# Kernel optimization log

Measured on AMD Instinct MI355X. Metric: run time of the kernel, lower is better.

The kernel has to match this reference:

```python
import jax, jax.numpy as jnp
import numpy as np
import math

EMBED_DIM = 1024
BATCH = 4
SEQ = 2048


def setup_inputs() -> dict:
    key = jax.random.key(0)
    ks = jax.random.split(key, 7)
    d = EMBED_DIM
    s = 1.0 / math.sqrt(d)
    x = jax.random.normal(ks[0], (BATCH, SEQ, d), dtype=jnp.float32)
    Wq = jax.random.normal(ks[1], (d, d), dtype=jnp.float32) * s
    Wk = jax.random.normal(ks[2], (d, d), dtype=jnp.float32) * s
    Wv = jax.random.normal(ks[3], (d, d), dtype=jnp.float32) * s
    bq = jax.random.normal(ks[4], (d,), dtype=jnp.float32) * 0.01
    bk = jax.random.normal(ks[5], (d,), dtype=jnp.float32) * 0.01
    bv = jax.random.normal(ks[6], (d,), dtype=jnp.float32) * 0.01
    return {"x": x, "Wq": Wq, "bq": bq, "Wk": Wk, "bk": bk, "Wv": Wv, "bv": bv}


def reference(x, Wq, bq, Wk, bk, Wv, bv):
    # q/k/v: [B, S, D] linear projections (weights stored as [in, out])
    q = jnp.einsum('bsd,de->bse', x, Wq) + bq
    k = jnp.einsum('bsd,de->bse', x, Wk) + bk
    v = jnp.einsum('bsd,de->bse', x, Wv) + bv
    scale = jnp.sqrt(jnp.asarray(x.shape[-1], dtype=x.dtype))
    # full O(S^2) score matrix, as in the original (non-fused) attention
    attn_scores = jnp.einsum('bqd,bkd->bqk', q, k) / scale
    attn_probs = jax.nn.softmax(attn_scores, axis=-1)
    # lxa.strassen(attn_probs, v) is a (Strassen) matmul: same math as matmul
    return jnp.einsum('bqk,bkd->bqd', attn_probs, v)
```

## Files before the change

### kernel.cpp

```cpp
#include <hip/hip_runtime.h>
#include <stdint.h>

#define SEQ 2048
#define DIM 1024
#define NB 4
#define MTOT (NB*SEQ)
#define QKVN (3*DIM)

typedef __attribute__((ext_vector_type(8))) short short8;
typedef __attribute__((ext_vector_type(4))) float f32x4;

__device__ __forceinline__ unsigned short f2b(float f) {
    union { float f; unsigned int u; } v; v.f = f;
    return (unsigned short)((v.u + 0x7FFFu + ((v.u >> 16) & 1u)) >> 16);
}

__device__ __forceinline__ void gload_lds16(const unsigned short* g, unsigned short* l) {
    __builtin_amdgcn_global_load_lds(
        (const __attribute__((address_space(1))) void*)g,
        (__attribute__((address_space(3))) void*)l, 16, 0, 0);
}

__device__ __forceinline__ short8 ds128(unsigned addr) {
    short8 r;
    asm volatile("ds_read_b128 %0, %1" : "=v"(r) : "v"(addr));
    return r;
}

#define FENCE_BARRIER do { asm volatile("" ::: "memory"); \
    __builtin_amdgcn_s_barrier(); asm volatile("" ::: "memory"); } while (0)

__device__ __forceinline__ int xcd_swz(int bid, int nwg) {
    if (nwg & 7) return bid;
    return (bid & 7) * (nwg >> 3) + (bid >> 3);
}


__global__ __launch_bounds__(256)
void cast_kernel(const float* __restrict__ in, unsigned short* __restrict__ out, int nchunk) {
    int i = blockIdx.x * 256 + threadIdx.x;
    if (i >= nchunk) return;
    float4 a = ((const float4*)in)[i*2];
    float4 b = ((const float4*)in)[i*2+1];
    union { unsigned short u[8]; uint4 v; } r;
    r.u[0]=f2b(a.x); r.u[1]=f2b(a.y); r.u[2]=f2b(a.z); r.u[3]=f2b(a.w);
    r.u[4]=f2b(b.x); r.u[5]=f2b(b.y); r.u[6]=f2b(b.z); r.u[7]=f2b(b.w);
    ((uint4*)out)[i] = r.v;
}

__global__ __launch_bounds__(256)
void transpose_cast_f32(const float* __restrict__ in, unsigned short* __restrict__ out, int R, int C) {
    __shared__ unsigned short tile[64][66];
    int tpc = C >> 6;
    int tr = (blockIdx.x / tpc) << 6;
    int tc = (blockIdx.x % tpc) << 6;
    int t = threadIdx.x;
    #pragma unroll
    for (int i = 0; i < 16; i++) {
        int idx = t + i*256;
        int r = idx >> 6, c = idx & 63;
        tile[r][c] = f2b(in[(size_t)(tr + r)*C + tc + c]);
    }
    __syncthreads();
    #pragma unroll
    for (int i = 0; i < 16; i++) {
        int idx = t + i*256;
        int r = idx >> 6, c = idx & 63;
        out[(size_t)(tc + r)*R + tr + c] = tile[c][r];
    }
}

__global__ __launch_bounds__(256)
void transpose_b16(const unsigned short* __restrict__ in0, size_t sIn, int ldin,
                   unsigned short* __restrict__ out0, size_t sOut, int ldout, int tpc) {
    const unsigned short* in = in0 + sIn * blockIdx.y;
    unsigned short* out = out0 + sOut * blockIdx.y;
    __shared__ unsigned short tile[64][66];
    int tr = ((int)blockIdx.x / tpc) << 6;
    int tc = ((int)blockIdx.x % tpc) << 6;
    int t = threadIdx.x;
    #pragma unroll
    for (int i = 0; i < 16; i++) {
        int idx = t + i*256;
        int r = idx >> 6, c = idx & 63;
        tile[r][c] = in[(size_t)(tr + r)*ldin + tc + c];
    }
    __syncthreads();
    #pragma unroll
    for (int i = 0; i < 16; i++) {
        int idx = t + i*256;
        int r = idx >> 6, c = idx & 63;
        out[(size_t)(tc + r)*ldout + tr + c] = tile[c][r];
    }
}

__global__ __launch_bounds__(256)
void bias_concat(const float* __restrict__ bq, const float* __restrict__ bk,
                 const float* __restrict__ bv, float* __restrict__ o) {
    int i = blockIdx.x*256 + threadIdx.x;
    float v = (i < DIM) ? bq[i] : ((i < 2*DIM) ? bk[i-DIM] : bv[i-2*DIM]);
    o[i] = v;
}


__device__ __forceinline__ void stage1(const unsigned short* __restrict__ Xb, int ldx,
                                       unsigned short* dstBase, int h, int k0,
                                       int tid, int wid) {
    int srow = tid >> 3;
    int scol = ((tid & 7) ^ (srow & 7)) << 3;
    const unsigned short* g = Xb + (size_t)(h*128 + srow)*ldx + k0 + scol;
    unsigned short* d = dstBase + h*8192 + wid*512;
    gload_lds16(g, d);
    gload_lds16(g + (size_t)64*ldx, d + 4096);
}

#define LDA_Q(BUF, QM) do { _Pragma("unroll") for (int mf = 0; mf < 4; ++mf) { \
    fa[mf][0] = ds128(As0 + (BUF)*32768u + (QM)*16384u + aRow + mf*2048u + c0); \
    fa[mf][1] = ds128(As0 + (BUF)*32768u + (QM)*16384u + aRow + mf*2048u + c1); } } while (0)

#define LDB_Q(BUF, QN) do { _Pragma("unroll") for (int nf = 0; nf < 2; ++nf) { \
    fb[nf][0] = ds128(Bs0 + (BUF)*32768u + (QN)*16384u + bRow + nf*2048u + c0); \
    fb[nf][1] = ds128(Bs0 + (BUF)*32768u + (QN)*16384u + bRow + nf*2048u + c1); } } while (0)

#define MMA_PH(QM, QN) do { \
    asm volatile("s_waitcnt lgkmcnt(0)" ::: "memory"); \
    __builtin_amdgcn_sched_barrier(0); \
    __builtin_amdgcn_s_setprio(1); \
    _Pragma("unroll") for (int mf = 0; mf < 4; ++mf) \
      _Pragma("unroll") for (int nf = 0; nf < 2; ++nf) \
        _Pragma("unroll") for (int ks = 0; ks < 2; ++ks) \
          acc[QM][QN][mf][nf] = __builtin_amdgcn_mfma_f32_16x16x32_bf16( \
              fa[mf][ks], fb[nf][ks], acc[QM][QN][mf][nf], 0, 0, 0); \
    __builtin_amdgcn_s_setprio(0); \
} while (0)

template<int MODE>
__global__ __launch_bounds__(512, 2)
void gemm8p(const unsigned short* __restrict__ A, int lda, size_t sA,
            const unsigned short* __restrict__ Bt, int ldb, size_t sB,
            const float* __restrict__ bias,
            void* __restrict__ Cout, int ldc, size_t sC,
            int N, int K)
{
    __shared__ __align__(16) unsigned short As[2][16384];
    __shared__ __align__(16) unsigned short Bs[2][16384];
    int nbn = N >> 8;
    int bid = xcd_swz((int)blockIdx.x, (int)gridDim.x);
    int bm = bid / nbn, bn = bid % nbn;
    int bz = blockIdx.y;
    int tid = threadIdx.x;
    int lane = tid & 63;
    int wid  = tid >> 6;
    int wm = (wid >> 2) & 1;
    int wn = wid & 3;
    int rlo = lane & 15;
    int shi = lane >> 4;

    unsigned As0 = (unsigned)(uintptr_t)&As[0][0];
    unsigned Bs0 = (unsigned)(uintptr_t)&Bs[0][0];
    unsigned c0 = (unsigned)(((shi     ^ rlo) & 7) * 16);
    unsigned c1 = (unsigned)((((4+shi) ^ rlo) & 7) * 16);
    unsigned aRow = (unsigned)((wm*64 + rlo) * 128);
    unsigned bRow = (unsigned)((wn*32 + rlo) * 128);

    f32x4 acc[2][2][4][2];
    #pragma unroll
    for (int a = 0; a < 2; a++)
        #pragma unroll
        for (int b = 0; b < 2; b++)
            #pragma unroll
            for (int c = 0; c < 4; c++)
                #pragma unroll
                for (int d = 0; d < 2; d++)
                    acc[a][b][c][d] = (f32x4){0.f,0.f,0.f,0.f};

    const unsigned short* Ab = A + sA*bz + (size_t)(bm*256)*lda;
    const unsigned short* Bb = Bt + sB*bz + (size_t)(bn*256)*ldb;

    stage1(Ab, lda, &As[0][0], 0, 0,  tid, wid);
    stage1(Bb, ldb, &Bs[0][0], 0, 0,  tid, wid);
    stage1(Ab, lda, &As[0][0], 1, 0,  tid, wid);
    stage1(Bb, ldb, &Bs[0][0], 1, 0,  tid, wid);
    stage1(Ab, lda, &As[1][0], 0, 64, tid, wid);
    stage1(Bb, ldb, &Bs[1][0], 1, 64, tid, wid);
    stage1(Ab, lda, &As[1][0], 1, 64, tid, wid);
    asm volatile("s_waitcnt vmcnt(6)" ::: "memory");
    FENCE_BARRIER;

    short8 fa[4][2], fb[2][2];
    int nt = K >> 6;
    int nit = nt >> 1;

    for (int it = 0; it < nit; ++it) {
        int kO  = (2*it + 1) << 6;
        int kE2 = (2*it + 2 < nt) ? (2*it + 2) << 6 : 0;
        int kO2 = (2*it + 3 < nt) ? (2*it + 3) << 6 : 0;

        LDA_Q(0, 0); LDB_Q(0, 0);
        stage1(Bb, ldb, &Bs[1][0], 0, kO, tid, wid);
        FENCE_BARRIER; MMA_PH(0, 0); FENCE_BARRIER;
        LDB_Q(0, 1);
        stage1(Ab, lda, &As[0][0], 0, kE2, tid, wid);
        FENCE_BARRIER; MMA_PH(0, 1); FENCE_BARRIER;
        LDA_Q(0, 1);
        stage1(Bb, ldb, &Bs[0][0], 1, kE2, tid, wid);
        FENCE_BARRIER; MMA_PH(1, 1); FENCE_BARRIER;
        LDB_Q(0, 0);
        stage1(Ab, lda, &As[0][0], 1, kE2, tid, wid);
        asm volatile("s_waitcnt vmcnt(6)" ::: "memory");
        FENCE_BARRIER; MMA_PH(1, 0); FENCE_BARRIER;
        LDA_Q(1, 0); LDB_Q(1, 0);
        stage1(Bb, ldb, &Bs[0][0], 0, kE2, tid, wid);
        FENCE_BARRIER; MMA_PH(0, 0); FENCE_BARRIER;
        LDB_Q(1, 1);
        stage1(Ab, lda, &As[1][0], 0, kO2, tid, wid);
        FENCE_BARRIER; MMA_PH(0, 1); FENCE_BARRIER;
        LDA_Q(1, 1);
        stage1(Bb, ldb, &Bs[1][0], 1, kO2, tid, wid);
        FENCE_BARRIER; MMA_PH(1, 1); FENCE_BARRIER;
        LDB_Q(1, 0);
        stage1(Ab, lda, &As[1][0], 1, kO2, tid, wid);
        asm volatile("s_waitcnt vmcnt(6)" ::: "memory");
        FENCE_BARRIER; MMA_PH(1, 0); FENCE_BARRIER;
    }

    asm volatile("s_waitcnt vmcnt(0)" ::: "memory");

    int r0 = shi << 2;
    unsigned short* Cu = (unsigned short*)Cout + sC*bz;
    float* Cf = (float*)Cout + sC*bz;
    #pragma unroll
    for (int qm = 0; qm < 2; ++qm)
        #pragma unroll
        for (int qn = 0; qn < 2; ++qn)
            #pragma unroll
            for (int mf = 0; mf < 4; ++mf)
                #pragma unroll
                for (int nf = 0; nf < 2; ++nf) {
                    int col = bn*256 + qn*128 + wn*32 + nf*16 + rlo;
                    float badd = (MODE == 0) ? bias[col] : 0.f;
                    #pragma unroll
                    for (int r = 0; r < 4; ++r) {
                        int row = bm*256 + qm*128 + wm*64 + mf*16 + r0 + r;
                        float v = acc[qm][qn][mf][nf][r];
                        if (MODE == 0) Cu[(size_t)row*ldc + col] = f2b(v + badd);
                        else           Cf[(size_t)row*ldc + col] = v;
                    }
                }
}

__global__ __launch_bounds__(256, 2)
void gemm_nt_pv(const unsigned short* __restrict__ A, int lda, size_t sA,
                const unsigned short* __restrict__ Bt, int ldb, size_t sB,
                float* __restrict__ Cout, int ldc, size_t sC,
                int N, int K)
{
    __shared__ __align__(16) unsigned short As[128][64];
    __shared__ __align__(16) unsigned short Bs[128][64];
    int nbn = N >> 7;
    int bid = xcd_swz((int)blockIdx.x, (int)gridDim.x);
    int bm = bid / nbn;
    int bn = bid % nbn;
    int bz = blockIdx.y;
    int tid = threadIdx.x;
    int lane = tid & 63;
    int wid  = tid >> 6;
    int wm = (wid >> 1) * 64, wn = (wid & 1) * 64;
    int lr = lane & 15;
    int lk = (lane >> 4) * 8;
    int srow = lane >> 3;
    int scol = (lane & 7) * 8;

    f32x4 acc[4][4];
    #pragma unroll
    for (int i = 0; i < 4; i++)
        #pragma unroll
        for (int j = 0; j < 4; j++) acc[i][j] = (f32x4){0.f,0.f,0.f,0.f};

    const unsigned short* Ab = A + sA*bz + (size_t)(bm*128)*lda;
    const unsigned short* Bb = Bt + sB*bz + (size_t)(bn*128)*ldb;

    for (int k0 = 0; k0 < K; k0 += 64) {
        #pragma unroll
        for (int r = 0; r < 4; r++) {
            int rowg = r*32 + wid*8;
            gload_lds16(Ab + (size_t)(rowg + srow)*lda + k0 + scol, &As[rowg][0]);
            gload_lds16(Bb + (size_t)(rowg + srow)*ldb + k0 + scol, &Bs[rowg][0]);
        }
        __syncthreads();
        #pragma unroll
        for (int ks = 0; ks < 2; ks++) {
            short8 af[4], bfr[4];
            #pragma unroll
            for (int mf = 0; mf < 4; mf++)
                af[mf] = *(const short8*)&As[wm + mf*16 + lr][ks*32 + lk];
            #pragma unroll
            for (int nf = 0; nf < 4; nf++)
                bfr[nf] = *(const short8*)&Bs[wn + nf*16 + lr][ks*32 + lk];
            #pragma unroll
            for (int mf = 0; mf < 4; mf++)
                #pragma unroll
                for (int nf = 0; nf < 4; nf++)
                    acc[mf][nf] = __builtin_amdgcn_mfma_f32_16x16x32_bf16(af[mf], bfr[nf], acc[mf][nf], 0, 0, 0);
        }
        __syncthreads();
    }

    int r0 = (lane >> 4) << 2;
    float* Cf = Cout + sC*bz;
    #pragma unroll
    for (int mf = 0; mf < 4; mf++)
        #pragma unroll
        for (int nf = 0; nf < 4; nf++) {
            int col = bn*128 + wn + nf*16 + lr;
            #pragma unroll
            for (int r = 0; r < 4; r++) {
                int row = bm*128 + wm + mf*16 + r0 + r;
                Cf[(size_t)row*ldc + col] = acc[mf][nf][r];
            }
        }
}

__global__ __launch_bounds__(256)
void softmax_kernel(float* __restrict__ S, float scl) {
    int row = blockIdx.x;
    float* srow = S + (size_t)row * SEQ;
    int t = threadIdx.x;
    float4 v0 = ((const float4*)srow)[t*2];
    float4 v1 = ((const float4*)srow)[t*2+1];
    float x[8] = {v0.x*scl,v0.y*scl,v0.z*scl,v0.w*scl,v1.x*scl,v1.y*scl,v1.z*scl,v1.w*scl};
    float m = fmaxf(fmaxf(fmaxf(x[0],x[1]),fmaxf(x[2],x[3])),
                    fmaxf(fmaxf(x[4],x[5]),fmaxf(x[6],x[7])));
    #pragma unroll
    for (int off = 32; off; off >>= 1) m = fmaxf(m, __shfl_xor(m, off));
    __shared__ float redm[4], reds[4];
    int w = t >> 6;
    if ((t & 63) == 0) redm[w] = m;
    __syncthreads();
    m = fmaxf(fmaxf(redm[0], redm[1]), fmaxf(redm[2], redm[3]));
    float e[8]; float s = 0.f;
    #pragma unroll
    for (int i = 0; i < 8; i++) { e[i] = __expf(x[i] - m); s += e[i]; }
    #pragma unroll
    for (int off = 32; off; off >>= 1) s += __shfl_xor(s, off);
    if ((t & 63) == 0) reds[w] = s;
    __syncthreads();
    float inv = 1.0f / (reds[0]+reds[1]+reds[2]+reds[3]);
    union { unsigned short u[8]; uint4 v; } r;
    #pragma unroll
    for (int i = 0; i < 8; i++) r.u[i] = f2b(e[i] * inv);
    ((uint4*)srow)[t] = r.v;
}

extern "C" void kernel_launch(void* const* d_in, const int* in_sizes, int n_in,
                              void* d_out, int out_size, void* d_ws, size_t ws_size,
                              hipStream_t stream)
{
    (void)in_sizes; (void)n_in; (void)out_size;
    const float* x  = (const float*)d_in[0];
    const float* Wq = (const float*)d_in[1];
    const float* bq = (const float*)d_in[2];
    const float* Wk = (const float*)d_in[3];
    const float* bk = (const float*)d_in[4];
    const float* Wv = (const float*)d_in[5];
    const float* bv = (const float*)d_in[6];
    float* out = (float*)d_out;

    unsigned short* qkv = (unsigned short*)d_ws;
    unsigned short* vt  = qkv + (size_t)MTOT*QKVN;
    float* biasc = (float*)(vt + (size_t)NB*DIM*SEQ);
    char* ovl = (char*)biasc + 65536;
    unsigned short* xb    = (unsigned short*)ovl;
    unsigned short* wqkvt = xb + (size_t)MTOT*DIM;
    float* scores = (float*)ovl;

    size_t base = (size_t)MTOT*QKVN*2 + (size_t)NB*DIM*SEQ*2 + 65536;
    int bpp = 1;
    if (base + 4*(size_t)SEQ*SEQ*4 <= ws_size) bpp = 4;
    else if (base + 2*(size_t)SEQ*SEQ*4 <= ws_size) bpp = 2;

    cast_kernel<<<MTOT*DIM/8/256, 256, 0, stream>>>(x, xb, MTOT*DIM/8);
    transpose_cast_f32<<<256, 256, 0, stream>>>(Wq, wqkvt,             DIM, DIM);
    transpose_cast_f32<<<256, 256, 0, stream>>>(Wk, wqkvt + DIM*DIM,   DIM, DIM);
    transpose_cast_f32<<<256, 256, 0, stream>>>(Wv, wqkvt + 2*DIM*DIM, DIM, DIM);
    bias_concat<<<QKVN/256, 256, 0, stream>>>(bq, bk, bv, biasc);

    gemm8p<0><<<dim3((MTOT/256)*(QKVN/256)), 512, 0, stream>>>(
        xb, DIM, 0, wqkvt, DIM, 0, biasc, qkv, QKVN, 0, QKVN, DIM);

    transpose_b16<<<dim3((SEQ/64)*(DIM/64), NB), 256, 0, stream>>>(
        qkv + 2*DIM, (size_t)SEQ*QKVN, QKVN, vt, (size_t)DIM*SEQ, SEQ, DIM/64);

    const float scl = 1.0f / 32.0f;
    for (int p = 0; p < NB; p += bpp) {
        const unsigned short* qp = qkv + (size_t)p*SEQ*QKVN;
        gemm8p<1><<<dim3((SEQ/256)*(SEQ/256), bpp), 512, 0, stream>>>(
            qp,       QKVN, (size_t)SEQ*QKVN,
            qp + DIM, QKVN, (size_t)SEQ*QKVN,
            nullptr, scores, SEQ, (size_t)SEQ*SEQ, SEQ, DIM);
        softmax_kernel<<<bpp*SEQ, 256, 0, stream>>>(scores, scl);
        gemm_nt_pv<<<dim3((SEQ/128)*(DIM/128), bpp), 256, 0, stream>>>(
            (const unsigned short*)scores, 2*SEQ, (size_t)SEQ*2*SEQ,
            vt + (size_t)p*DIM*SEQ,        SEQ,   (size_t)DIM*SEQ,
            out + (size_t)p*SEQ*DIM, DIM, (size_t)SEQ*DIM, DIM, SEQ);
    }
}
```

Before: 193.1 us.

## Software-pipeline LDS fragment reads with MFMA phases using double register buffers

```diff
diff --git a/kernel.cpp b/kernel.cpp
--- a/kernel.cpp
+++ b/kernel.cpp
@@ -114,24 +114,25 @@
     gload_lds16(g + (size_t)64*ldx, d + 4096);
 }
 
-#define LDA_Q(BUF, QM) do { _Pragma("unroll") for (int mf = 0; mf < 4; ++mf) { \
-    fa[mf][0] = ds128(As0 + (BUF)*32768u + (QM)*16384u + aRow + mf*2048u + c0); \
-    fa[mf][1] = ds128(As0 + (BUF)*32768u + (QM)*16384u + aRow + mf*2048u + c1); } } while (0)
-
-#define LDB_Q(BUF, QN) do { _Pragma("unroll") for (int nf = 0; nf < 2; ++nf) { \
-    fb[nf][0] = ds128(Bs0 + (BUF)*32768u + (QN)*16384u + bRow + nf*2048u + c0); \
-    fb[nf][1] = ds128(Bs0 + (BUF)*32768u + (QN)*16384u + bRow + nf*2048u + c1); } } while (0)
-
-#define MMA_PH(QM, QN) do { \
-    asm volatile("s_waitcnt lgkmcnt(0)" ::: "memory"); \
+#define RD_A(DST, BUF, QM) do { _Pragma("unroll") for (int mf = 0; mf < 4; ++mf) { \
+    DST[mf][0] = ds128(As0 + (BUF)*32768u + (QM)*16384u + aRow + mf*2048u + c0);   \
+    DST[mf][1] = ds128(As0 + (BUF)*32768u + (QM)*16384u + aRow + mf*2048u + c1); } } while (0)
+
+#define RD_B(DST, BUF, QN) do { _Pragma("unroll") for (int nf = 0; nf < 2; ++nf) { \
+    DST[nf][0] = ds128(Bs0 + (BUF)*32768u + (QN)*16384u + bRow + nf*2048u + c0);   \
+    DST[nf][1] = ds128(Bs0 + (BUF)*32768u + (QN)*16384u + bRow + nf*2048u + c1); } } while (0)
+
+#define MMA16(FA, FB, QM, QN) do { \
     __builtin_amdgcn_sched_barrier(0); \
     __builtin_amdgcn_s_setprio(1); \
     _Pragma("unroll") for (int mf = 0; mf < 4; ++mf) \
       _Pragma("unroll") for (int nf = 0; nf < 2; ++nf) \
         _Pragma("unroll") for (int ks = 0; ks < 2; ++ks) \
           acc[QM][QN][mf][nf] = __builtin_amdgcn_mfma_f32_16x16x32_bf16( \
-              fa[mf][ks], fb[nf][ks], acc[QM][QN][mf][nf], 0, 0, 0); \
+              FA[mf][ks], FB[nf][ks], acc[QM][QN][mf][nf], 0, 0, 0); \
     __builtin_amdgcn_s_setprio(0); \
+    asm volatile("s_waitcnt lgkmcnt(0)" ::: "memory"); \
+    __builtin_amdgcn_sched_barrier(0); \
 } while (0)
 
 template<int MODE>
@@ -177,6 +178,11 @@
     const unsigned short* Ab = A + sA*bz + (size_t)(bm*256)*lda;
     const unsigned short* Bb = Bt + sB*bz + (size_t)(bn*256)*ldb;
 
+    short8 faA[4][2], faB[4][2];
+    short8 fb0X[2][2];
+    short8 fb0Y[2][2];
+    short8 fb1[2][2];
+
     stage1(Ab, lda, &As[0][0], 0, 0,  tid, wid);
     stage1(Bb, ldb, &Bs[0][0], 0, 0,  tid, wid);
     stage1(Ab, lda, &As[0][0], 1, 0,  tid, wid);
@@ -184,44 +190,57 @@
     stage1(Ab, lda, &As[1][0], 0, 64, tid, wid);
     stage1(Bb, ldb, &Bs[1][0], 1, 64, tid, wid);
     stage1(Ab, lda, &As[1][0], 1, 64, tid, wid);
+    stage1(Bb, ldb, &Bs[1][0], 0, 64, tid, wid);
+    __builtin_amdgcn_sched_barrier(0);
     asm volatile("s_waitcnt vmcnt(6)" ::: "memory");
     FENCE_BARRIER;
-
-    short8 fa[4][2], fb[2][2];
+    RD_A(faA, 0, 0); RD_B(fb0X, 0, 0);
+    __builtin_amdgcn_sched_barrier(0);
+    asm volatile("s_waitcnt lgkmcnt(0)" ::: "memory");
+    __builtin_amdgcn_sched_barrier(0);
+    FENCE_BARRIER;
+
     int nt = K >> 6;
     int nit = nt >> 1;
 
     for (int it = 0; it < nit; ++it) {
-        int kO  = (2*it + 1) << 6;
         int kE2 = (2*it + 2 < nt) ? (2*it + 2) << 6 : 0;
         int kO2 = (2*it + 3 < nt) ? (2*it + 3) << 6 : 0;
 
-        LDA_Q(0, 0); LDB_Q(0, 0);
-        stage1(Bb, ldb, &Bs[1][0], 0, kO, tid, wid);
-        FENCE_BARRIER; MMA_PH(0, 0); FENCE_BARRIER;
-        LDB_Q(0, 1);
+        RD_B(fb1, 0, 1);
+        MMA16(faA, fb0X, 0, 0);
         stage1(Ab, lda, &As[0][0], 0, kE2, tid, wid);
-        FENCE_BARRIER; MMA_PH(0, 1); FENCE_BARRIER;
-        LDA_Q(0, 1);
+        FENCE_BARRIER;
+        RD_A(faB, 0, 1);
+        MMA16(faA, fb1, 0, 1);
         stage1(Bb, ldb, &Bs[0][0], 1, kE2, tid, wid);
-        FENCE_BARRIER; MMA_PH(1, 1); FENCE_BARRIER;
-        LDB_Q(0, 0);
+        FENCE_BARRIER;
+        MMA16(faB, fb1, 1, 1);
         stage1(Ab, lda, &As[0][0], 1, kE2, tid, wid);
+        __builtin_amdgcn_sched_barrier(0);
         asm volatile("s_waitcnt vmcnt(6)" ::: "memory");
-        FENCE_BARRIER; MMA_PH(1, 0); FENCE_BARRIER;
-        LDA_Q(1, 0); LDB_Q(1, 0);
+        FENCE_BARRIER;
+        RD_A(faA, 1, 0); RD_B(fb0Y, 1, 0);
+        MMA16(faB, fb0X, 1, 0);
         stage1(Bb, ldb, &Bs[0][0], 0, kE2, tid, wid);
-        FENCE_BARRIER; MMA_PH(0, 0); FENCE_BARRIER;
-        LDB_Q(1, 1);
+        FENCE_BARRIER;
+        RD_B(fb1, 1, 1);
+        MMA16(faA, fb0Y, 0, 0);
         stage1(Ab, lda, &As[1][0], 0, kO2, tid, wid);
-        FENCE_BARRIER; MMA_PH(0, 1); FENCE_BARRIER;
-        LDA_Q(1, 1);
+        FENCE_BARRIER;
+        RD_A(faB, 1, 1);
+        MMA16(faA, fb1, 0, 1);
         stage1(Bb, ldb, &Bs[1][0], 1, kO2, tid, wid);
-        FENCE_BARRIER; MMA_PH(1, 1); FENCE_BARRIER;
-        LDB_Q(1, 0);
+        FENCE_BARRIER;
+        MMA16(faB, fb1, 1, 1);
         stage1(Ab, lda, &As[1][0], 1, kO2, tid, wid);
+        __builtin_amdgcn_sched_barrier(0);
         asm volatile("s_waitcnt vmcnt(6)" ::: "memory");
-        FENCE_BARRIER; MMA_PH(1, 0); FENCE_BARRIER;
+        FENCE_BARRIER;
+        RD_A(faA, 0, 0); RD_B(fb0X, 0, 0);
+        MMA16(faB, fb0Y, 1, 0);
+        stage1(Bb, ldb, &Bs[1][0], 0, kO2, tid, wid);
+        FENCE_BARRIER;
     }
 
     asm volatile("s_waitcnt vmcnt(0)" ::: "memory");
```

Result: slower. 288.4 us (+49.3%).
